# Optimization experiments

Hardware: AMD Instinct MI355X
Metric: run time of the kernel (lower is better)

## Reference

```python
import jax, jax.numpy as jnp
import numpy as np

N_NODES = 100000
N_EDGES = 3200000
N_SAMPLES = 8
EPS_CONST = 1e-8


def setup_inputs() -> dict:
    key = jax.random.key(0)
    k1, k2, k3, k4 = jax.random.split(key, 4)
    mu = jax.random.normal(k1, (N_NODES,), dtype=jnp.float32)
    log_sigma = jax.random.normal(k2, (N_NODES,), dtype=jnp.float32)
    eps = jax.random.normal(k3, (N_SAMPLES, N_NODES), dtype=jnp.float32)
    edges = jax.random.randint(k4, (N_EDGES, 2), 0, N_NODES, dtype=jnp.int64)
    return {"mu": mu, "log_sigma": log_sigma, "eps": eps, "edges": edges, "n_samples": N_SAMPLES}


def reference(mu, log_sigma, eps, edges, n_samples):
    # c_samples: [S, N]
    c = mu + jnp.exp(log_sigma) * eps
    ci = c[:, edges[:, 0]]  # [S, E] gather
    cj = c[:, edges[:, 1]]  # [S, E] gather
    p = jax.nn.sigmoid(ci * cj)
    # original: sum over edges of mean over samples
    loglik = jnp.log(p + EPS_CONST).mean(axis=0).sum()
    return loglik
```

## Files before the change

### kernel.cpp

```cpp
#include <hip/hip_runtime.h>
#include <hip/hip_fp16.h>


typedef unsigned int u32x4 __attribute__((ext_vector_type(4)));
typedef int          i32x4 __attribute__((ext_vector_type(4)));

__device__ __forceinline__ float edge_term(u32x4 A, u32x4 B) {
    float t[8];
#pragma unroll
    for (int k = 0; k < 4; ++k) {
        __half2 a = __builtin_bit_cast(__half2, A[k]);
        __half2 b = __builtin_bit_cast(__half2, B[k]);
        __half2 xh = __hmul2(a, b);
        float2 xf = __half22float2(xh);
        t[2 * k]     = fminf(__expf(-xf.x), 1.0e8f);
        t[2 * k + 1] = fminf(__expf(-xf.y), 1.0e8f);
    }
    float p0 = 1.0f + t[0];
    p0 = __builtin_fmaf(p0, t[1], p0);
    p0 = __builtin_fmaf(p0, t[2], p0);
    p0 = __builtin_fmaf(p0, t[3], p0);
    float p1 = 1.0f + t[4];
    p1 = __builtin_fmaf(p1, t[5], p1);
    p1 = __builtin_fmaf(p1, t[6], p1);
    p1 = __builtin_fmaf(p1, t[7], p1);
    return __logf(p0) + __logf(p1);
}

__global__ void compute_c_h8(const float* __restrict__ mu,
                             const float* __restrict__ ls,
                             const float* __restrict__ eps,
                             __half2* __restrict__ c, int N,
                             float* __restrict__ out, int out_size) {
    if (blockIdx.x == gridDim.x - 1) {
        for (int i = threadIdx.x; i < out_size; i += blockDim.x) out[i] = 0.0f;
        return;
    }
    int n = blockIdx.x * blockDim.x + threadIdx.x;
    if (n >= N) return;
    float m  = mu[n];
    float sg = __expf(ls[n]);
    float v[8];
#pragma unroll
    for (int s = 0; s < 8; ++s) v[s] = m + sg * eps[(size_t)s * N + n];
    __half2* dst = c + (size_t)n * 4;
#pragma unroll
    for (int s = 0; s < 4; ++s) dst[s] = __floats2half2_rn(v[2 * s], v[2 * s + 1]);
}

__global__ void __launch_bounds__(256, 8)
edge_loglik_s8(const i32x4* __restrict__ ep, const u32x4* __restrict__ c,
               float* __restrict__ out, long long E, float neg_inv_s) {
    long long tid    = (long long)blockIdx.x * blockDim.x + threadIdx.x;
    long long stride = (long long)gridDim.x * blockDim.x;
    float acc = 0.0f;
    long long P = E >> 1;

    for (long long q = tid; q < P; q += 2 * stride) {
        long long q1 = q + stride;
        bool has1 = q1 < P;
        i32x4 e0 = __builtin_nontemporal_load(ep + q);
        i32x4 e1 = has1 ? __builtin_nontemporal_load(ep + q1) : e0;
        u32x4 a0 = c[e0.x], b0 = c[e0.y], d0 = c[e0.z], f0 = c[e0.w];
        u32x4 a1 = c[e1.x], b1 = c[e1.y], d1 = c[e1.z], f1 = c[e1.w];
        float s = edge_term(a0, b0) + edge_term(d0, f0);
        if (has1) s += edge_term(a1, b1) + edge_term(d1, f1);
        acc += s;
    }
    if ((E & 1) && tid == 0) {
        const int2* el = (const int2*)ep;
        int2 ij = el[E - 1];
        acc += edge_term(c[ij.x], c[ij.y]);
    }

#pragma unroll
    for (int off = 32; off > 0; off >>= 1) acc += __shfl_down(acc, off, 64);
    __shared__ float wsum[4];
    int lane = threadIdx.x & 63;
    int wid  = threadIdx.x >> 6;
    if (lane == 0) wsum[wid] = acc;
    __syncthreads();
    if (threadIdx.x == 0) {
        float s = 0.0f;
        for (int w = 0; w < (int)(blockDim.x >> 6); ++w) s += wsum[w];
        atomicAdd(out, s * neg_inv_s);
    }
}

__global__ void compute_c_gen(const float* __restrict__ mu, const float* __restrict__ ls,
                              const float* __restrict__ eps, __half* __restrict__ c,
                              int N, int S, float* __restrict__ out, int out_size) {
    if (blockIdx.x == gridDim.x - 1) {
        for (int i = threadIdx.x; i < out_size; i += blockDim.x) out[i] = 0.0f;
        return;
    }
    int n = blockIdx.x * blockDim.x + threadIdx.x;
    if (n >= N) return;
    float m = mu[n], sg = __expf(ls[n]);
    for (int s = 0; s < S; ++s) c[(size_t)n * S + s] = __float2half(m + sg * eps[(size_t)s * N + n]);
}
__global__ void edge_loglik_gen(const int* __restrict__ ed, const __half* __restrict__ c,
                                float* __restrict__ out, long long E, int S, float neg_inv_s) {
    long long tid = (long long)blockIdx.x * blockDim.x + threadIdx.x;
    long long stride = (long long)gridDim.x * blockDim.x;
    float acc = 0.0f;
    for (long long e = tid; e < E; e += stride) {
        long long i = ed[2 * e], j = ed[2 * e + 1];
        for (int s = 0; s < S; ++s) {
            float x = __half2float(c[i * S + s]) * __half2float(c[j * S + s]);
            acc += __logf(1.0f + fminf(__expf(-x), 1.0e8f));
        }
    }
#pragma unroll
    for (int off = 32; off > 0; off >>= 1) acc += __shfl_down(acc, off, 64);
    __shared__ float wsum[8];
    int lane = threadIdx.x & 63, wid = threadIdx.x >> 6;
    if (lane == 0) wsum[wid] = acc;
    __syncthreads();
    if (threadIdx.x == 0) {
        float s = 0.0f;
        for (int w = 0; w < (int)(blockDim.x >> 6); ++w) s += wsum[w];
        atomicAdd(out, s * neg_inv_s);
    }
}

extern "C" void kernel_launch(void* const* d_in, const int* in_sizes, int n_in,
                              void* d_out, int out_size, void* d_ws, size_t ws_size,
                              hipStream_t stream) {
    const float* mu  = (const float*)d_in[0];
    const float* ls  = (const float*)d_in[1];
    const float* eps = (const float*)d_in[2];
    const int* edges = (const int*)d_in[3];

    int       N = in_sizes[0];
    int       S = in_sizes[2] / N;
    long long E = (long long)in_sizes[3] / 2;

    __half* c  = (__half*)d_ws;
    float* out = (float*)d_out;
    size_t sz_c = (size_t)N * S * sizeof(__half);
    float neg_inv_s = -1.0f / (float)S;

    int cblocks = (N + 255) / 256 + 1;

    if (S == 8 && ws_size >= sz_c) {
        compute_c_h8<<<cblocks, 256, 0, stream>>>(mu, ls, eps, (__half2*)c, N, out, out_size);
        edge_loglik_s8<<<2048, 256, 0, stream>>>((const i32x4*)edges, (const u32x4*)c,
                                                 out, E, neg_inv_s);
    } else {
        compute_c_gen<<<cblocks, 256, 0, stream>>>(mu, ls, eps, c, N, S, out, out_size);
        edge_loglik_gen<<<2048, 256, 0, stream>>>(edges, c, out, E, S, neg_inv_s);
    }
}
```

Baseline: 46.93 us.

## Prefetch gathered node rows into LDS with double-buffered async global_load_lds

Replaces the two-pair-per-thread edge kernel with a software-pipelined kernel that gathers the two c rows for each edge directly into per-wave LDS buffers via global_load_lds. Edge indices are prefetched two iterations ahead and the LDS buffers are double-buffered, with manual vmcnt waits. This aims to overlap the random gather latency with compute, but it reduces per-thread memory-level parallelism and relies on hand-managed waitcnt ordering. A simple one-edge-per-thread fallback is kept for small E.

```diff
diff --git a/kernel.cpp b/kernel.cpp
--- a/kernel.cpp
+++ b/kernel.cpp
@@ -3,7 +3,10 @@
 
 
 typedef unsigned int u32x4 __attribute__((ext_vector_type(4)));
-typedef int          i32x4 __attribute__((ext_vector_type(4)));
+
+#define TPB   256
+#define NBLK  2048
+#define TTLL  ((long long)NBLK * TPB)
 
 __device__ __forceinline__ float edge_term(u32x4 A, u32x4 B) {
     float t[8];
@@ -48,36 +51,77 @@
     for (int s = 0; s < 4; ++s) dst[s] = __floats2half2_rn(v[2 * s], v[2 * s + 1]);
 }
 
+#define GLOAD_LDS(gp, lp)                                                        \
+    __builtin_amdgcn_global_load_lds(                                            \
+        (const __attribute__((address_space(1))) void*)(gp),                     \
+        (__attribute__((address_space(3))) void*)(lp), 16, 0, 0)
+
+__global__ void __launch_bounds__(TPB, 8)
+edge_loglik_lds(const int2* __restrict__ edges, const u32x4* __restrict__ c,
+                float* __restrict__ out, long long E, int NIT, float neg_inv_s) {
+    __shared__ char smem[TPB / 64 * 4096];
+    long long tid  = (long long)blockIdx.x * TPB + threadIdx.x;
+    int  lane  = threadIdx.x & 63;
+    int  wid   = threadIdx.x >> 6;
+    char* wb   = smem + wid * 4096;
+    float acc  = 0.0f;
+
+    long long i0 = tid < E ? tid : (E - 1);
+    int2 e_cur  = edges[i0];
+    GLOAD_LDS(c + e_cur.x, wb);
+    GLOAD_LDS(c + e_cur.y, wb + 1024);
+    long long i1 = tid + TTLL;
+    int2 e_next = edges[i1 < E ? i1 : (E - 1)];
+
+    for (int t = 0; t + 1 < NIT; ++t) {
+        long long i2 = tid + (long long)(t + 2) * TTLL;
+        int2 e_n2 = edges[i2 < E ? i2 : (E - 1)];
+        char* nb = wb + ((t + 1) & 1) * 2048;
+        GLOAD_LDS(c + e_next.x, nb);
+        GLOAD_LDS(c + e_next.y, nb + 1024);
+        asm volatile("s_waitcnt vmcnt(3)" ::: "memory");
+        char* cb = wb + (t & 1) * 2048;
+        u32x4 A = *(const u32x4*)(cb + lane * 16);
+        u32x4 B = *(const u32x4*)(cb + 1024 + lane * 16);
+        if (tid + (long long)t * TTLL < E) acc += edge_term(A, B);
+        e_cur = e_next;
+        e_next = e_n2;
+    }
+    asm volatile("s_waitcnt vmcnt(0)" ::: "memory");
+    {
+        int t = NIT - 1;
+        char* cb = wb + (t & 1) * 2048;
+        u32x4 A = *(const u32x4*)(cb + lane * 16);
+        u32x4 B = *(const u32x4*)(cb + 1024 + lane * 16);
+        if (tid + (long long)t * TTLL < E) acc += edge_term(A, B);
+    }
+
+#pragma unroll
+    for (int off = 32; off > 0; off >>= 1) acc += __shfl_down(acc, off, 64);
+    __shared__ float wsum[4];
+    if (lane == 0) wsum[wid] = acc;
+    __syncthreads();
+    if (threadIdx.x == 0) {
+        float s = 0.0f;
+        for (int w = 0; w < TPB / 64; ++w) s += wsum[w];
+        atomicAdd(out, s * neg_inv_s);
+    }
+}
+
 __global__ void __launch_bounds__(256, 8)
-edge_loglik_s8(const i32x4* __restrict__ ep, const u32x4* __restrict__ c,
-               float* __restrict__ out, long long E, float neg_inv_s) {
+edge_loglik_direct(const int2* __restrict__ el, const u32x4* __restrict__ c,
+                   float* __restrict__ out, long long E, float neg_inv_s) {
     long long tid    = (long long)blockIdx.x * blockDim.x + threadIdx.x;
     long long stride = (long long)gridDim.x * blockDim.x;
     float acc = 0.0f;
-    long long P = E >> 1;
-
-    for (long long q = tid; q < P; q += 2 * stride) {
-        long long q1 = q + stride;
-        bool has1 = q1 < P;
-        i32x4 e0 = __builtin_nontemporal_load(ep + q);
-        i32x4 e1 = has1 ? __builtin_nontemporal_load(ep + q1) : e0;
-        u32x4 a0 = c[e0.x], b0 = c[e0.y], d0 = c[e0.z], f0 = c[e0.w];
-        u32x4 a1 = c[e1.x], b1 = c[e1.y], d1 = c[e1.z], f1 = c[e1.w];
-        float s = edge_term(a0, b0) + edge_term(d0, f0);
-        if (has1) s += edge_term(a1, b1) + edge_term(d1, f1);
-        acc += s;
-    }
-    if ((E & 1) && tid == 0) {
-        const int2* el = (const int2*)ep;
-        int2 ij = el[E - 1];
+    for (long long e = tid; e < E; e += stride) {
+        int2 ij = el[e];
         acc += edge_term(c[ij.x], c[ij.y]);
     }
-
 #pragma unroll
     for (int off = 32; off > 0; off >>= 1) acc += __shfl_down(acc, off, 64);
     __shared__ float wsum[4];
-    int lane = threadIdx.x & 63;
-    int wid  = threadIdx.x >> 6;
+    int lane = threadIdx.x & 63, wid = threadIdx.x >> 6;
     if (lane == 0) wsum[wid] = acc;
     __syncthreads();
     if (threadIdx.x == 0) {
@@ -142,11 +186,17 @@
     float neg_inv_s = -1.0f / (float)S;
 
     int cblocks = (N + 255) / 256 + 1;
+    int NIT = (int)((E + TTLL - 1) / TTLL);
 
     if (S == 8 && ws_size >= sz_c) {
         compute_c_h8<<<cblocks, 256, 0, stream>>>(mu, ls, eps, (__half2*)c, N, out, out_size);
-        edge_loglik_s8<<<2048, 256, 0, stream>>>((const i32x4*)edges, (const u32x4*)c,
-                                                 out, E, neg_inv_s);
+        if (NIT >= 2) {
+            edge_loglik_lds<<<NBLK, TPB, 0, stream>>>((const int2*)edges, (const u32x4*)c,
+                                                      out, E, NIT, neg_inv_s);
+        } else {
+            edge_loglik_direct<<<2048, 256, 0, stream>>>((const int2*)edges, (const u32x4*)c,
+                                                         out, E, neg_inv_s);
+        }
     } else {
         compute_c_gen<<<cblocks, 256, 0, stream>>>(mu, ls, eps, c, N, S, out, out_size);
         edge_loglik_gen<<<2048, 256, 0, stream>>>(edges, c, out, E, S, neg_inv_s);
```

Result: slower. 51.00 us (+8.7%).
